# Performance work log

Hardware: AMD Instinct MI355X
Metric: run time of the kernel (lower is better)

The kernel has to match this reference:

```python
import jax, jax.numpy as jnp
import numpy as np


def setup_inputs() -> dict:
    key = jax.random.key(0)
    k1, k2, k3 = jax.random.split(key, 3)
    B, C, H, W = 32, 1, 512, 512
    input1 = jax.random.normal(k1, (B, C, H, W), dtype=jnp.float32)
    input2 = jax.random.normal(k2, (B, C, H, W), dtype=jnp.float32)
    # binary segmentation mask (float, as it multiplies float activations)
    mask = (jax.random.uniform(k3, (B, C, H, W)) > 0.5).astype(jnp.float32)
    return {"input1": input1, "input2": input2, "mask": mask}


def reference(input1, input2, mask):
    # logit=True branch of CosineContrastiveLoss_NoExp
    x1 = jax.nn.sigmoid(input1)  # [B,C,H,W]
    x2 = jax.nn.sigmoid(input2)
    # positive similarity per sample (mask applied once, as in original)
    num_pos = jnp.sqrt(jnp.sum((mask * x1 * x2) ** 2, axis=(1, 2, 3)))
    den_pos = (jnp.sqrt(jnp.sum((mask * x1) ** 2, axis=(1, 2, 3)))
               * jnp.sqrt(jnp.sum((mask * x2) ** 2, axis=(1, 2, 3))))
    sim_pos = num_pos / den_pos  # [B]
    # negative similarities: pairwise over batch, per channel.
    # sum_{h,w} (x1[b1]*x2[b2])^2 = <x1[b1]^2, x2[b2]^2> -> single einsum,
    # replacing the O(B^2) Python loop of tiny reductions.
    sq1 = x1 * x1
    sq2 = x2 * x2
    num = jnp.sqrt(jnp.einsum('bchw,dchw->bdc', sq1, sq2))  # [B,B,C]
    n1 = jnp.sqrt(jnp.sum(sq1, axis=(2, 3)))  # [B,C]
    n2 = jnp.sqrt(jnp.sum(sq2, axis=(2, 3)))  # [B,C]
    sim = num / (n1[:, None, :] * n2[None, :, :])  # [B,B,C]
    B = sim.shape[0]
    off_diag = (1.0 - jnp.eye(B, dtype=sim.dtype))[:, :, None]
    sim_neg = jnp.sum(sim * off_diag, axis=1)  # [B,C]
    # broadcasting [B] against [B,C]; with C==1 this yields [B,B] as in torch
    loss = -jnp.log(sim_pos / (sim_pos + sim_neg))
    return jnp.mean(loss)
```

## Files before the change

### kernel.cpp

```cpp
#include <hip/hip_runtime.h>
#include <math.h>

#define BATCH 32
#define HW (512*512)
#define TILE 256
#define NT (HW / TILE)
#define RS 264
#define SLICE 1184
#define RED2N 9472

typedef __attribute__((ext_vector_type(8))) short bf16x8;
typedef __attribute__((ext_vector_type(4))) float f32x4;

__device__ __forceinline__ float fsigmoid(float x) {
    float e = __builtin_amdgcn_exp2f(-x * 1.44269504088896340736f);
    return __builtin_amdgcn_rcpf(1.0f + e);
}

__device__ __forceinline__ unsigned pkbf(float a, float b) {
    unsigned ua = __float_as_uint(a);
    ua = (ua + 0x7fffu + ((ua >> 16) & 1u)) >> 16;
    unsigned ub = __float_as_uint(b);
    ub = (ub + 0x7fffu + ((ub >> 16) & 1u)) & 0xffff0000u;
    return ua | ub;
}

__global__ __launch_bounds__(256, 4) void cos_loss_main(
    const float* __restrict__ x1, const float* __restrict__ x2,
    const float* __restrict__ mk, float* __restrict__ ws, int ns)
{
    __shared__ __align__(16) short smem[2 * BATCH * RS];

    const int t = threadIdx.x;
    const int w = t >> 6;
    const int l = t & 63;

    if (blockIdx.x == 0 && t == 0) {
        unsigned* cnt = (unsigned*)(ws + (size_t)ns * SLICE + RED2N);
        *cnt = 0u;
    }

    short* S1 = smem;
    short* S2 = smem + BATCH * RS;

    const int arow = w * 8 + (l >> 3);
    const int a8   = (l & 7) * 4;
    const int q    = l >> 4;
    const int fr   = l & 15;

    f32x4 acc00 = {0.f,0.f,0.f,0.f}, acc01 = {0.f,0.f,0.f,0.f};
    f32x4 acc10 = {0.f,0.f,0.f,0.f}, acc11 = {0.f,0.f,0.f,0.f};
    float n1 = 0.f, n2 = 0.f, pp = 0.f, p1 = 0.f, p2 = 0.f;

    for (int tile = blockIdx.x; tile < NT; tile += ns) {
        const int base = tile * TILE;
        __syncthreads();

        const unsigned rbase = (unsigned)arow * HW + base + a8;
        short* w1 = S1 + arow * RS + a8;
        short* w2 = S2 + arow * RS + a8;
        #pragma unroll 2
        for (int it = 0; it < 8; ++it) {
            float4 v1 = *(const float4*)(x1 + rbase + it * 32);
            float4 v2 = *(const float4*)(x2 + rbase + it * 32);
            float4 vm = *(const float4*)(mk + rbase + it * 32);
            float4 q1, q2;
            { float s = fsigmoid(v1.x); q1.x = s*s; }
            { float s = fsigmoid(v1.y); q1.y = s*s; }
            { float s = fsigmoid(v1.z); q1.z = s*s; }
            { float s = fsigmoid(v1.w); q1.w = s*s; }
            { float s = fsigmoid(v2.x); q2.x = s*s; }
            { float s = fsigmoid(v2.y); q2.y = s*s; }
            { float s = fsigmoid(v2.z); q2.z = s*s; }
            { float s = fsigmoid(v2.w); q2.w = s*s; }
            n1 += (q1.x + q1.y) + (q1.z + q1.w);
            n2 += (q2.x + q2.y) + (q2.z + q2.w);
            p1 = fmaf(vm.x, q1.x, fmaf(vm.y, q1.y, fmaf(vm.z, q1.z, fmaf(vm.w, q1.w, p1))));
            p2 = fmaf(vm.x, q2.x, fmaf(vm.y, q2.y, fmaf(vm.z, q2.z, fmaf(vm.w, q2.w, p2))));
            pp = fmaf(vm.x, q1.x*q2.x, fmaf(vm.y, q1.y*q2.y,
                 fmaf(vm.z, q1.z*q2.z, fmaf(vm.w, q1.w*q2.w, pp))));
            uint2 u1; u1.x = pkbf(q1.x, q1.y); u1.y = pkbf(q1.z, q1.w);
            uint2 u2; u2.x = pkbf(q2.x, q2.y); u2.y = pkbf(q2.z, q2.w);
            *(uint2*)(w1 + it * 32) = u1;
            *(uint2*)(w2 + it * 32) = u2;
        }
        __syncthreads();

        const int kb = fr * RS + w * 64;
        #pragma unroll
        for (int ks = 0; ks < 2; ++ks) {
            bf16x8 a0 = *(const bf16x8*)(S1 + kb + ks * 32 + q * 8);
            bf16x8 a1 = *(const bf16x8*)(S1 + kb + 16 * RS + ks * 32 + q * 8);
            bf16x8 b0 = *(const bf16x8*)(S2 + kb + ks * 32 + q * 8);
            bf16x8 b1 = *(const bf16x8*)(S2 + kb + 16 * RS + ks * 32 + q * 8);
            acc00 = __builtin_amdgcn_mfma_f32_16x16x32_bf16(a0, b0, acc00, 0, 0, 0);
            acc01 = __builtin_amdgcn_mfma_f32_16x16x32_bf16(a0, b1, acc01, 0, 0, 0);
            acc10 = __builtin_amdgcn_mfma_f32_16x16x32_bf16(a1, b0, acc10, 0, 0, 0);
            acc11 = __builtin_amdgcn_mfma_f32_16x16x32_bf16(a1, b1, acc11, 0, 0, 0);
        }
    }

    float* slice = ws + (size_t)blockIdx.x * SLICE;

    #pragma unroll
    for (int off = 1; off < 8; off <<= 1) {
        n1 += __shfl_xor(n1, off);
        n2 += __shfl_xor(n2, off);
        pp += __shfl_xor(pp, off);
        p1 += __shfl_xor(p1, off);
        p2 += __shfl_xor(p2, off);
    }
    if ((l & 7) == 0) {
        slice[1024 +       arow] = n1;
        slice[1024 +  32 + arow] = n2;
        slice[1024 +  64 + arow] = pp;
        slice[1024 +  96 + arow] = p1;
        slice[1024 + 128 + arow] = p2;
    }

    __syncthreads();
    float* Gm = (float*)smem;
    {
        const int gb = w * 1024;
        #pragma unroll
        for (int r2 = 0; r2 < 4; ++r2) {
            Gm[gb + (     q*4 + r2) * 32 +      fr] = acc00[r2];
            Gm[gb + (     q*4 + r2) * 32 + 16 + fr] = acc01[r2];
            Gm[gb + (16 + q*4 + r2) * 32 +      fr] = acc10[r2];
            Gm[gb + (16 + q*4 + r2) * 32 + 16 + fr] = acc11[r2];
        }
    }
    __syncthreads();
    #pragma unroll
    for (int r2 = 0; r2 < 4; ++r2) {
        int e = r2 * 256 + t;
        slice[e] = ((Gm[e] + Gm[1024 + e]) + (Gm[2048 + e] + Gm[3072 + e]));
    }
}

__global__ __launch_bounds__(256) void cos_loss_tail(
    float* __restrict__ ws, int ns, float* __restrict__ out)
{
    float* red2 = ws + (size_t)ns * SLICE;
    unsigned* cnt = (unsigned*)(red2 + RED2N);

    const int t  = threadIdx.x;
    const int ib = blockIdx.x;
    const int kc = blockIdx.y;
    const int e  = ib * 32 + (t & 31);
    const int kq = t >> 5;

    const int k0 = (kc * ns) >> 3, k1 = ((kc + 1) * ns) >> 3;
    float s = 0.f;
    for (int k = k0 + kq; k < k1; k += 8)
        s += ws[(size_t)k * SLICE + e];

    __shared__ float part[8][33];
    part[kq][t & 31] = s;
    __syncthreads();
    if (t < 32) {
        float v = 0.f;
        #pragma unroll
        for (int j = 0; j < 8; ++j) v += part[j][t];
        red2[kc * SLICE + ib * 32 + t] = v;
    }
    __syncthreads();

    __shared__ int lastFlag;
    if (t == 0) {
        __threadfence();
        unsigned old = atomicAdd(cnt, 1u);
        lastFlag = (old == gridDim.x * gridDim.y - 1u);
    }
    __syncthreads();
    if (!lastFlag) return;
    __threadfence();

    __shared__ float red[SLICE];
    for (int e2 = t; e2 < SLICE; e2 += 256) {
        float v = 0.f;
        #pragma unroll
        for (int c = 0; c < 8; ++c) v += red2[c * SLICE + e2];
        red[e2] = v;
    }
    __syncthreads();

    __shared__ float spv[32], snv[32];
    if (t < 32)
        spv[t] = sqrtf(red[1024 + 64 + t]) /
                 (sqrtf(red[1024 + 96 + t]) * sqrtf(red[1024 + 128 + t]));
    __syncthreads();

    #pragma unroll
    for (int rep = 0; rep < 4; ++rep) {
        int idx = rep * 256 + t;
        int b = idx >> 5, d = idx & 31;
        float sim = 0.f;
        if (b != d)
            sim = sqrtf(red[idx]) /
                  (sqrtf(red[1024 + b]) * sqrtf(red[1024 + 32 + d]));
        #pragma unroll
        for (int off = 1; off < 32; off <<= 1) sim += __shfl_xor(sim, off);
        if ((t & 31) == 0) snv[b] = sim;
    }
    __syncthreads();

    float ls = 0.f;
    #pragma unroll
    for (int rep = 0; rep < 4; ++rep) {
        int idx = rep * 256 + t;
        int i = idx >> 5, j = idx & 31;
        ls += -logf(spv[j] / (spv[j] + snv[i]));
    }
    #pragma unroll
    for (int off = 1; off < 64; off <<= 1) ls += __shfl_xor(ls, off);
    __shared__ float wsum[4];
    if ((t & 63) == 0) wsum[t >> 6] = ls;
    __syncthreads();
    if (t == 0)
        out[0] = ((wsum[0] + wsum[1]) + (wsum[2] + wsum[3])) * (1.0f / 1024.0f);
}

extern "C" void kernel_launch(void* const* d_in, const int* in_sizes, int n_in,
                              void* d_out, int out_size, void* d_ws, size_t ws_size,
                              hipStream_t stream)
{
    const float* x1 = (const float*)d_in[0];
    const float* x2 = (const float*)d_in[1];
    const float* mk = (const float*)d_in[2];
    float* out = (float*)d_out;
    float* ws  = (float*)d_ws;

    long wsf = (long)(ws_size / sizeof(float));
    int ns = (int)((wsf - RED2N - 16) / SLICE);
    if (ns > NT) ns = NT;
    if (ns < 1) ns = 1;

    cos_loss_main<<<ns, 256, 0, stream>>>(x1, x2, mk, ws, ns);
    cos_loss_tail<<<dim3(37, 8), 256, 0, stream>>>(ws, ns, out);
}
```

Measured before the change: 40.14 us.

## Remap load lanes to contiguous row spans and unroll tail reduction

Each wavefront now loads a full 256-element row span per batch row, so one instruction covers 1KB of contiguous memory instead of eight 128-byte pieces. The loop over the 8 rows is fully unrolled, which puts more loads in flight. This needs per-row accumulator arrays (40 registers) and a full 64-lane shuffle reduction at the end. Separately, the tail kernel's strided partial-sum loop is unrolled into four independent accumulators to expose more memory-level parallelism.

```diff
diff --git a/kernel.cpp b/kernel.cpp
--- a/kernel.cpp
+++ b/kernel.cpp
@@ -43,27 +43,27 @@
     short* S1 = smem;
     short* S2 = smem + BATCH * RS;
 
-    const int arow = w * 8 + (l >> 3);
-    const int a8   = (l & 7) * 4;
-    const int q    = l >> 4;
-    const int fr   = l & 15;
+    const int pos = l * 4;
+    const int q   = l >> 4;
+    const int fr  = l & 15;
 
     f32x4 acc00 = {0.f,0.f,0.f,0.f}, acc01 = {0.f,0.f,0.f,0.f};
     f32x4 acc10 = {0.f,0.f,0.f,0.f}, acc11 = {0.f,0.f,0.f,0.f};
-    float n1 = 0.f, n2 = 0.f, pp = 0.f, p1 = 0.f, p2 = 0.f;
+    float n1a[8], n2a[8], ppa[8], p1a[8], p2a[8];
+    #pragma unroll
+    for (int k = 0; k < 8; ++k) { n1a[k]=0.f; n2a[k]=0.f; ppa[k]=0.f; p1a[k]=0.f; p2a[k]=0.f; }
 
     for (int tile = blockIdx.x; tile < NT; tile += ns) {
         const int base = tile * TILE;
         __syncthreads();
 
-        const unsigned rbase = (unsigned)arow * HW + base + a8;
-        short* w1 = S1 + arow * RS + a8;
-        short* w2 = S2 + arow * RS + a8;
-        #pragma unroll 2
-        for (int it = 0; it < 8; ++it) {
-            float4 v1 = *(const float4*)(x1 + rbase + it * 32);
-            float4 v2 = *(const float4*)(x2 + rbase + it * 32);
-            float4 vm = *(const float4*)(mk + rbase + it * 32);
+        #pragma unroll
+        for (int k = 0; k < 8; ++k) {
+            const int row = w * 8 + k;
+            const unsigned gidx = (unsigned)row * HW + base + pos;
+            float4 v1 = *(const float4*)(x1 + gidx);
+            float4 v2 = *(const float4*)(x2 + gidx);
+            float4 vm = *(const float4*)(mk + gidx);
             float4 q1, q2;
             { float s = fsigmoid(v1.x); q1.x = s*s; }
             { float s = fsigmoid(v1.y); q1.y = s*s; }
@@ -73,16 +73,16 @@
             { float s = fsigmoid(v2.y); q2.y = s*s; }
             { float s = fsigmoid(v2.z); q2.z = s*s; }
             { float s = fsigmoid(v2.w); q2.w = s*s; }
-            n1 += (q1.x + q1.y) + (q1.z + q1.w);
-            n2 += (q2.x + q2.y) + (q2.z + q2.w);
-            p1 = fmaf(vm.x, q1.x, fmaf(vm.y, q1.y, fmaf(vm.z, q1.z, fmaf(vm.w, q1.w, p1))));
-            p2 = fmaf(vm.x, q2.x, fmaf(vm.y, q2.y, fmaf(vm.z, q2.z, fmaf(vm.w, q2.w, p2))));
-            pp = fmaf(vm.x, q1.x*q2.x, fmaf(vm.y, q1.y*q2.y,
-                 fmaf(vm.z, q1.z*q2.z, fmaf(vm.w, q1.w*q2.w, pp))));
+            n1a[k] += (q1.x + q1.y) + (q1.z + q1.w);
+            n2a[k] += (q2.x + q2.y) + (q2.z + q2.w);
+            p1a[k] = fmaf(vm.x, q1.x, fmaf(vm.y, q1.y, fmaf(vm.z, q1.z, fmaf(vm.w, q1.w, p1a[k]))));
+            p2a[k] = fmaf(vm.x, q2.x, fmaf(vm.y, q2.y, fmaf(vm.z, q2.z, fmaf(vm.w, q2.w, p2a[k]))));
+            ppa[k] = fmaf(vm.x, q1.x*q2.x, fmaf(vm.y, q1.y*q2.y,
+                     fmaf(vm.z, q1.z*q2.z, fmaf(vm.w, q1.w*q2.w, ppa[k]))));
             uint2 u1; u1.x = pkbf(q1.x, q1.y); u1.y = pkbf(q1.z, q1.w);
             uint2 u2; u2.x = pkbf(q2.x, q2.y); u2.y = pkbf(q2.z, q2.w);
-            *(uint2*)(w1 + it * 32) = u1;
-            *(uint2*)(w2 + it * 32) = u2;
+            *(uint2*)(S1 + row * RS + pos) = u1;
+            *(uint2*)(S2 + row * RS + pos) = u2;
         }
         __syncthreads();
 
@@ -103,19 +103,24 @@
     float* slice = ws + (size_t)blockIdx.x * SLICE;
 
     #pragma unroll
-    for (int off = 1; off < 8; off <<= 1) {
-        n1 += __shfl_xor(n1, off);
-        n2 += __shfl_xor(n2, off);
-        pp += __shfl_xor(pp, off);
-        p1 += __shfl_xor(p1, off);
-        p2 += __shfl_xor(p2, off);
-    }
-    if ((l & 7) == 0) {
-        slice[1024 +       arow] = n1;
-        slice[1024 +  32 + arow] = n2;
-        slice[1024 +  64 + arow] = pp;
-        slice[1024 +  96 + arow] = p1;
-        slice[1024 + 128 + arow] = p2;
+    for (int k = 0; k < 8; ++k) {
+        float v0 = n1a[k], v1 = n2a[k], v2 = ppa[k], v3 = p1a[k], v4 = p2a[k];
+        #pragma unroll
+        for (int off = 1; off < 64; off <<= 1) {
+            v0 += __shfl_xor(v0, off);
+            v1 += __shfl_xor(v1, off);
+            v2 += __shfl_xor(v2, off);
+            v3 += __shfl_xor(v3, off);
+            v4 += __shfl_xor(v4, off);
+        }
+        if (l == 0) {
+            const int row = w * 8 + k;
+            slice[1024 +       row] = v0;
+            slice[1024 +  32 + row] = v1;
+            slice[1024 +  64 + row] = v2;
+            slice[1024 +  96 + row] = v3;
+            slice[1024 + 128 + row] = v4;
+        }
     }
 
     __syncthreads();
@@ -151,9 +156,16 @@
     const int kq = t >> 5;
 
     const int k0 = (kc * ns) >> 3, k1 = ((kc + 1) * ns) >> 3;
-    float s = 0.f;
-    for (int k = k0 + kq; k < k1; k += 8)
-        s += ws[(size_t)k * SLICE + e];
+    float s0 = 0.f, s1 = 0.f, s2 = 0.f, s3 = 0.f;
+    int k = k0 + kq;
+    for (; k + 24 < k1; k += 32) {
+        s0 += ws[(size_t)(k     ) * SLICE + e];
+        s1 += ws[(size_t)(k +  8) * SLICE + e];
+        s2 += ws[(size_t)(k + 16) * SLICE + e];
+        s3 += ws[(size_t)(k + 24) * SLICE + e];
+    }
+    for (; k < k1; k += 8) s0 += ws[(size_t)k * SLICE + e];
+    float s = (s0 + s1) + (s2 + s3);
 
     __shared__ float part[8][33];
     part[kq][t & 31] = s;
```

Result: slower. 49.61 us (+23.6%).

## Double-buffer LDS tiles with register prefetch and cap grid at 1024 blocks

Applied to the files above, without the earlier changes.

Halves the tile width and adds two LDS buffers so each iteration needs only one barrier. Global loads for the next half-tile are issued while the current half is put through sigmoid and packed into LDS, hiding memory latency. The grid is capped at 1024 blocks so the tail kernel has fewer per-block slices to reduce. The tail's reduction loop is also unrolled into four independent accumulators. The trade-offs are more registers held for prefetched data and twice as many loop iterations per block.

```diff
diff --git a/kernel.cpp b/kernel.cpp
--- a/kernel.cpp
+++ b/kernel.cpp
@@ -3,14 +3,18 @@
 
 #define BATCH 32
 #define HW (512*512)
-#define TILE 256
+#define TILE 128
 #define NT (HW / TILE)
-#define RS 264
+#define RS 136
+#define ARRSH (BATCH * RS)
+#define BUFSH (2 * ARRSH)
 #define SLICE 1184
 #define RED2N 9472
 
 typedef __attribute__((ext_vector_type(8))) short bf16x8;
 typedef __attribute__((ext_vector_type(4))) float f32x4;
+
+struct HalfT { float4 v1[2], v2[2], vm[2]; };
 
 __device__ __forceinline__ float fsigmoid(float x) {
     float e = __builtin_amdgcn_exp2f(-x * 1.44269504088896340736f);
@@ -29,7 +33,7 @@
     const float* __restrict__ x1, const float* __restrict__ x2,
     const float* __restrict__ mk, float* __restrict__ ws, int ns)
 {
-    __shared__ __align__(16) short smem[2 * BATCH * RS];
+    __shared__ __align__(16) short smem[2 * BUFSH];
 
     const int t = threadIdx.x;
     const int w = t >> 6;
@@ -39,31 +43,32 @@
         unsigned* cnt = (unsigned*)(ws + (size_t)ns * SLICE + RED2N);
         *cnt = 0u;
     }
-
-    short* S1 = smem;
-    short* S2 = smem + BATCH * RS;
 
     const int arow = w * 8 + (l >> 3);
     const int a8   = (l & 7) * 4;
     const int q    = l >> 4;
     const int fr   = l & 15;
 
+    const unsigned rowbase = (unsigned)arow * HW + a8;
+    const int      woff    = arow * RS + a8;
+
     f32x4 acc00 = {0.f,0.f,0.f,0.f}, acc01 = {0.f,0.f,0.f,0.f};
     f32x4 acc10 = {0.f,0.f,0.f,0.f}, acc11 = {0.f,0.f,0.f,0.f};
     float n1 = 0.f, n2 = 0.f, pp = 0.f, p1 = 0.f, p2 = 0.f;
 
-    for (int tile = blockIdx.x; tile < NT; tile += ns) {
-        const int base = tile * TILE;
-        __syncthreads();
-
-        const unsigned rbase = (unsigned)arow * HW + base + a8;
-        short* w1 = S1 + arow * RS + a8;
-        short* w2 = S2 + arow * RS + a8;
-        #pragma unroll 2
-        for (int it = 0; it < 8; ++it) {
-            float4 v1 = *(const float4*)(x1 + rbase + it * 32);
-            float4 v2 = *(const float4*)(x2 + rbase + it * 32);
-            float4 vm = *(const float4*)(mk + rbase + it * 32);
+    auto LD = [&](HalfT& H, int tile, int h) {
+        const unsigned g = rowbase + (unsigned)tile * TILE + h * 64;
+        #pragma unroll
+        for (int i = 0; i < 2; ++i) {
+            H.v1[i] = *(const float4*)(x1 + g + i * 32);
+            H.v2[i] = *(const float4*)(x2 + g + i * 32);
+            H.vm[i] = *(const float4*)(mk + g + i * 32);
+        }
+    };
+    auto PROC = [&](const HalfT& H, int h, short* B1, short* B2) {
+        #pragma unroll
+        for (int i = 0; i < 2; ++i) {
+            float4 v1 = H.v1[i], v2 = H.v2[i], vm = H.vm[i];
             float4 q1, q2;
             { float s = fsigmoid(v1.x); q1.x = s*s; }
             { float s = fsigmoid(v1.y); q1.y = s*s; }
@@ -81,23 +86,37 @@
                  fmaf(vm.z, q1.z*q2.z, fmaf(vm.w, q1.w*q2.w, pp))));
             uint2 u1; u1.x = pkbf(q1.x, q1.y); u1.y = pkbf(q1.z, q1.w);
             uint2 u2; u2.x = pkbf(q2.x, q2.y); u2.y = pkbf(q2.z, q2.w);
-            *(uint2*)(w1 + it * 32) = u1;
-            *(uint2*)(w2 + it * 32) = u2;
+            *(uint2*)(B1 + woff + (h * 2 + i) * 32) = u1;
+            *(uint2*)(B2 + woff + (h * 2 + i) * 32) = u2;
         }
-        __syncthreads();
-
-        const int kb = fr * RS + w * 64;
-        #pragma unroll
-        for (int ks = 0; ks < 2; ++ks) {
-            bf16x8 a0 = *(const bf16x8*)(S1 + kb + ks * 32 + q * 8);
-            bf16x8 a1 = *(const bf16x8*)(S1 + kb + 16 * RS + ks * 32 + q * 8);
-            bf16x8 b0 = *(const bf16x8*)(S2 + kb + ks * 32 + q * 8);
-            bf16x8 b1 = *(const bf16x8*)(S2 + kb + 16 * RS + ks * 32 + q * 8);
-            acc00 = __builtin_amdgcn_mfma_f32_16x16x32_bf16(a0, b0, acc00, 0, 0, 0);
-            acc01 = __builtin_amdgcn_mfma_f32_16x16x32_bf16(a0, b1, acc01, 0, 0, 0);
-            acc10 = __builtin_amdgcn_mfma_f32_16x16x32_bf16(a1, b0, acc10, 0, 0, 0);
-            acc11 = __builtin_amdgcn_mfma_f32_16x16x32_bf16(a1, b1, acc11, 0, 0, 0);
-        }
+    };
+
+    HalfT A, B;
+    int p = 0;
+    int tile = blockIdx.x;
+    if (tile < NT) LD(A, tile, 0);
+    for (; tile < NT; tile += ns) {
+        short* B1 = smem + p * BUFSH;
+        short* B2 = B1 + ARRSH;
+
+        LD(B, tile, 1);
+        PROC(A, 0, B1, B2);
+        if (tile + ns < NT) LD(A, tile + ns, 0);
+        PROC(B, 1, B1, B2);
+
+        asm volatile("s_waitcnt lgkmcnt(0)" ::: "memory");
+        __builtin_amdgcn_s_barrier();
+
+        const int kb = fr * RS + w * 32 + q * 8;
+        bf16x8 a0 = *(const bf16x8*)(B1 + kb);
+        bf16x8 a1 = *(const bf16x8*)(B1 + kb + 16 * RS);
+        bf16x8 b0 = *(const bf16x8*)(B2 + kb);
+        bf16x8 b1 = *(const bf16x8*)(B2 + kb + 16 * RS);
+        acc00 = __builtin_amdgcn_mfma_f32_16x16x32_bf16(a0, b0, acc00, 0, 0, 0);
+        acc01 = __builtin_amdgcn_mfma_f32_16x16x32_bf16(a0, b1, acc01, 0, 0, 0);
+        acc10 = __builtin_amdgcn_mfma_f32_16x16x32_bf16(a1, b0, acc10, 0, 0, 0);
+        acc11 = __builtin_amdgcn_mfma_f32_16x16x32_bf16(a1, b1, acc11, 0, 0, 0);
+        p ^= 1;
     }
 
     float* slice = ws + (size_t)blockIdx.x * SLICE;
@@ -151,9 +170,16 @@
     const int kq = t >> 5;
 
     const int k0 = (kc * ns) >> 3, k1 = ((kc + 1) * ns) >> 3;
-    float s = 0.f;
-    for (int k = k0 + kq; k < k1; k += 8)
-        s += ws[(size_t)k * SLICE + e];
+    float s0 = 0.f, s1 = 0.f, s2 = 0.f, s3 = 0.f;
+    int k = k0 + kq;
+    for (; k + 24 < k1; k += 32) {
+        s0 += ws[(size_t)(k     ) * SLICE + e];
+        s1 += ws[(size_t)(k +  8) * SLICE + e];
+        s2 += ws[(size_t)(k + 16) * SLICE + e];
+        s3 += ws[(size_t)(k + 24) * SLICE + e];
+    }
+    for (; k < k1; k += 8) s0 += ws[(size_t)k * SLICE + e];
+    float s = (s0 + s1) + (s2 + s3);
 
     __shared__ float part[8][33];
     part[kq][t & 31] = s;
@@ -233,7 +259,7 @@
 
     long wsf = (long)(ws_size / sizeof(float));
     int ns = (int)((wsf - RED2N - 16) / SLICE);
-    if (ns > NT) ns = NT;
+    if (ns > 1024) ns = 1024;
     if (ns < 1) ns = 1;
 
     cos_loss_main<<<ns, 256, 0, stream>>>(x1, x2, mk, ws, ns);
```

After: 40.53 us (median of 2 runs). Within noise of the previous version (+1.0%).
